# Kernel tuning notes

Hardware: AMD Instinct MI355X
Metric: run time of the kernel (lower is better)

The kernel has to match this reference:

```python
import jax, jax.numpy as jnp
import numpy as np

# ---- static configuration (mirrors init_kwargs) ----
B, V, C, NH, HD = 1, 6, 256, 8, 32     # batch, views, embed, heads, head_dim
Z, L, P = 4, 4, 2                       # z-ref points, fmap levels, ref points
BEV_H, BEV_W = 80, 80
Q = BEV_H * BEV_W
IMG_H, IMG_W = 480, 800
LEVEL_SHAPES = [(60, 100), (30, 50), (15, 25), (8, 13)]
S = sum(h * w for h, w in LEVEL_SHAPES)
RES = 0.512
OFFSET_SCALE = 1.0
FF = 512


def layer_norm(x, g, b):
    m = jnp.mean(x, -1, keepdims=True)
    v = jnp.var(x, -1, keepdims=True)
    return (x - m) / jnp.sqrt(v + 1e-5) * g + b


def _bev_grid():
    xs = (jnp.arange(BEV_W) + 0.5) / BEV_W
    ys = (jnp.arange(BEV_H) + 0.5) / BEV_H
    gy, gx = jnp.meshgrid(ys, xs, indexing='ij')
    ref = jnp.stack([gx.reshape(-1), gy.reshape(-1)], -1)        # (Q,2) normalized xy
    world = (ref - 0.5) * jnp.array([BEV_W * RES, BEV_H * RES])  # (Q,2) ego-frame meters
    return ref, world


def deform_sample(value, H, W, loc):
    """Bilinear sampling. value: (N, H*W, NH, HD); loc: (N, Qn, NH, PP, 2) in [0,1].
    Returns (N, Qn, NH, PP, HD); out-of-bounds samples contribute zero."""
    v = jnp.moveaxis(value, 2, 1)                                # (N, NH, HW, HD)
    x = loc[..., 0] * W - 0.5
    y = loc[..., 1] * H - 0.5
    x0 = jnp.floor(x); y0 = jnp.floor(y)
    lx, ly = x - x0, y - y0
    x0 = x0.astype(jnp.int32); y0 = y0.astype(jnp.int32)
    gather = jax.vmap(jax.vmap(lambda vt, it: vt[it]))           # over (N, NH)
    def corner(xi, yi, w):
        ok = ((xi >= 0) & (xi < W) & (yi >= 0) & (yi < H)).astype(value.dtype)
        idx = jnp.clip(yi, 0, H - 1) * W + jnp.clip(xi, 0, W - 1)
        g = gather(v, jnp.moveaxis(idx, 2, 1))                   # (N,NH,Qn,PP,HD)
        return jnp.moveaxis(g, 1, 2) * (w * ok)[..., None]
    return (corner(x0, y0, (1 - lx) * (1 - ly)) + corner(x0 + 1, y0, lx * (1 - ly))
            + corner(x0, y0 + 1, (1 - lx) * ly) + corner(x0 + 1, y0 + 1, lx * ly))


def _forward(bev_queries, bev_histories, multiscale_fmaps, transition_matrices, z_refs,
             cam_proj_matrices, Wv_t, Woff_t, boff_t, Ww_t, bw_t, Wo_t, bo_t, ln1_g, ln1_b,
             Wv_s, Woff_s, boff_s, Ww_s, bw_s, Wo_s, bo_s, ln2_g, ln2_b,
             W1, b1, W2, b2, ln3_g, ln3_b):
    ref, world = _bev_grid()
    q = bev_queries
    # ---------- temporal self-attention (deformable over current + warped history) ----------
    vcur = (q @ Wv_t).reshape(B, Q, NH, HD)
    vhist = (bev_histories @ Wv_t).reshape(B, Q, NH, HD)
    off_t = (q @ Woff_t + boff_t).reshape(B, Q, NH, 2, P, 2) * OFFSET_SCALE
    w_t = jax.nn.softmax((q @ Ww_t + bw_t).reshape(B, Q, NH, 2 * P), -1).reshape(B, Q, NH, 2, P)
    ext = jnp.array([BEV_W * RES, BEV_H * RES], jnp.float32)
    wh = jnp.concatenate([world, jnp.ones((Q, 1), jnp.float32)], -1)     # (Q,3)
    warped = jnp.einsum('bij,qj->bqi', transition_matrices, wh)          # (B,Q,3)
    ref_hist = warped[..., :2] / warped[..., 2:3] / ext + 0.5            # (B,Q,2)
    norm_bev = jnp.array([BEV_W, BEV_H], jnp.float32)
    loc_c = ref[None, :, None, None, :] + off_t[:, :, :, 0] / norm_bev
    loc_h = ref_hist[:, :, None, None, :] + off_t[:, :, :, 1] / norm_bev
    s_c = deform_sample(vcur, BEV_H, BEV_W, loc_c)                       # (B,Q,NH,P,HD)
    s_h = deform_sample(vhist, BEV_H, BEV_W, loc_h)
    out_t = (jnp.einsum('bqhp,bqhpd->bqhd', w_t[:, :, :, 0], s_c)
             + jnp.einsum('bqhp,bqhpd->bqhd', w_t[:, :, :, 1], s_h))
    out1 = out_t.reshape(B, Q, C) @ Wo_t + bo_t
    out2 = layer_norm(out1 + q, ln1_g, ln1_b)
    # ---------- spatial cross-attention (multi-view multi-scale deformable) ----------
    val = (multiscale_fmaps @ Wv_s).reshape(B * V, S, NH, HD)
    pts = jnp.concatenate([
        jnp.broadcast_to(world[:, None, :], (Q, Z, 2)),
        jnp.broadcast_to(z_refs[None, :, None], (Q, Z, 1)),
        jnp.ones((Q, Z, 1), jnp.float32)], -1)                           # (Q,Z,4) homogeneous
    uvd = jnp.einsum('vij,qzj->vqzi', cam_proj_matrices, pts)            # (V,Q,Z,3)
    d = uvd[..., 2]
    un = uvd[..., 0] / jnp.maximum(d, 1e-5) / IMG_W
    vn = uvd[..., 1] / jnp.maximum(d, 1e-5) / IMG_H
    valid = ((d > 1e-5) & (un >= 0) & (un <= 1) & (vn >= 0) & (vn <= 1)).astype(q.dtype)
    refuv = jnp.stack([un, vn], -1)                                      # (V,Q,Z,2)
    off_s = (out2 @ Woff_s + boff_s).reshape(B, Q, NH, Z, L, P, 2) * OFFSET_SCALE
    w_s = jax.nn.softmax((out2 @ Ww_s + bw_s).reshape(B, Q, NH, Z * L * P), -1)
    w_s = w_s.reshape(B, Q, NH, Z, L, P)
    acc = jnp.zeros((B, Q, NH, HD), q.dtype)
    start = 0
    for l, (Hl, Wl) in enumerate(LEVEL_SHAPES):
        vl = val[:, start:start + Hl * Wl]
        start += Hl * Wl
        loc = (refuv[None, :, :, None, :, None, :]
               + off_s[:, None, :, :, :, l] / jnp.array([Wl, Hl], jnp.float32))
        loc = jnp.broadcast_to(loc, (B, V, Q, NH, Z, P, 2)).reshape(B * V, Q, NH, Z * P, 2)
        samp = deform_sample(vl, Hl, Wl, loc).reshape(B, V, Q, NH, Z, P, HD)
        wl = w_s[:, None, :, :, :, l] * valid[None, :, :, None, :, None]
        acc = acc + jnp.einsum('bvqhzp,bvqhzpd->bqhd', wl, samp)
    count = jnp.maximum(valid.sum((0, 2)), 1.0)                          # (Q,) hit count
    out3 = (acc / count[None, :, None, None]).reshape(B, Q, C) @ Wo_s + bo_s
    out4 = layer_norm(out3 + out2, ln2_g, ln2_b)
    # ---------- feed-forward ----------
    out5 = jax.nn.relu(out4 @ W1 + b1) @ W2 + b2
    return layer_norm(out5 + out4, ln3_g, ln3_b)


def setup_inputs() -> dict:
    key = jax.random.key(0)
    ks = iter(jax.random.split(key, 40))
    def rn(shape, s=1.0):
        return jax.random.normal(next(ks), shape, jnp.float32) * s
    sc = 1.0 / float(np.sqrt(C))
    inp = {}
    inp['bev_queries'] = rn((B, Q, C), 0.1)
    inp['bev_histories'] = rn((B, Q, C), 0.1)
    inp['multiscale_fmaps'] = rn((B, V, S, C), 0.1)
    th = 0.02
    T = np.array([[np.cos(th), -np.sin(th), 0.5],
                  [np.sin(th), np.cos(th), 0.1],
                  [0.0, 0.0, 1.0]], np.float32)
    inp['transition_matrices'] = jnp.tile(jnp.asarray(T)[None], (B, 1, 1))
    inp['z_refs'] = jnp.linspace(-5.0, 3.0, Z).astype(jnp.float32)
    K = np.array([[400.0, 0.0, IMG_W / 2], [0.0, 400.0, IMG_H / 2], [0.0, 0.0, 1.0]], np.float32)
    Ps = []
    for vi in range(V):
        a = 2 * np.pi * vi / V
        Rt = np.zeros((3, 4), np.float32)
        Rt[0, :3] = [-np.sin(a), np.cos(a), 0.0]   # camera right
        Rt[1, :3] = [0.0, 0.0, -1.0]               # camera down
        Rt[2, :3] = [np.cos(a), np.sin(a), 0.0]    # camera forward
        Ps.append(K @ Rt)
    inp['cam_proj_matrices'] = jnp.asarray(np.stack(Ps))
    # temporal self-attention params
    inp['Wv_t'] = rn((C, C), sc)
    inp['Woff_t'] = rn((C, NH * 2 * P * 2), sc * 0.1)
    inp['boff_t'] = jnp.zeros((NH * 2 * P * 2,), jnp.float32)
    inp['Ww_t'] = rn((C, NH * 2 * P), sc)
    inp['bw_t'] = jnp.zeros((NH * 2 * P,), jnp.float32)
    inp['Wo_t'] = rn((C, C), sc)
    inp['bo_t'] = jnp.zeros((C,), jnp.float32)
    inp['ln1_g'] = jnp.ones((C,), jnp.float32)
    inp['ln1_b'] = jnp.zeros((C,), jnp.float32)
    # spatial cross-attention params
    inp['Wv_s'] = rn((C, C), sc)
    inp['Woff_s'] = rn((C, NH * Z * L * P * 2), sc * 0.1)
    inp['boff_s'] = jnp.zeros((NH * Z * L * P * 2,), jnp.float32)
    inp['Ww_s'] = rn((C, NH * Z * L * P), sc)
    inp['bw_s'] = jnp.zeros((NH * Z * L * P,), jnp.float32)
    inp['Wo_s'] = rn((C, C), sc)
    inp['bo_s'] = jnp.zeros((C,), jnp.float32)
    inp['ln2_g'] = jnp.ones((C,), jnp.float32)
    inp['ln2_b'] = jnp.zeros((C,), jnp.float32)
    # FFN params
    inp['W1'] = rn((C, FF), sc)
    inp['b1'] = jnp.zeros((FF,), jnp.float32)
    inp['W2'] = rn((FF, C), 1.0 / float(np.sqrt(FF)))
    inp['b2'] = jnp.zeros((C,), jnp.float32)
    inp['ln3_g'] = jnp.ones((C,), jnp.float32)
    inp['ln3_b'] = jnp.zeros((C,), jnp.float32)
    # static shape descriptors (treated as compile-time constants)
    inp['bev_spatial_shape'] = np.array([[BEV_H, BEV_W]], np.int64)
    inp['multiscale_fmap_shapes'] = np.array(LEVEL_SHAPES, np.int64)
    inp['img_spatial_shape'] = np.array([[IMG_H, IMG_W]], np.int64)
    return inp


def reference(bev_queries, bev_histories, multiscale_fmaps, transition_matrices, z_refs,
              cam_proj_matrices, Wv_t, Woff_t, boff_t, Ww_t, bw_t, Wo_t, bo_t, ln1_g, ln1_b,
              Wv_s, Woff_s, boff_s, Ww_s, bw_s, Wo_s, bo_s, ln2_g, ln2_b,
              W1, b1, W2, b2, ln3_g, ln3_b,
              bev_spatial_shape, multiscale_fmap_shapes, img_spatial_shape):
    return _forward(bev_queries, bev_histories, multiscale_fmaps, transition_matrices, z_refs,
                    cam_proj_matrices, Wv_t, Woff_t, boff_t, Ww_t, bw_t, Wo_t, bo_t, ln1_g, ln1_b,
                    Wv_s, Woff_s, boff_s, Ww_s, bw_s, Wo_s, bo_s, ln2_g, ln2_b,
                    W1, b1, W2, b2, ln3_g, ln3_b)
```

## Files before the change

kernel.cpp:

```cpp
#include <hip/hip_runtime.h>
#include <hip/hip_bf16.h>
#include <hip/hip_fp16.h>

typedef unsigned short u16;
typedef unsigned int u32;
typedef __attribute__((ext_vector_type(8))) short bf16x8;
typedef __attribute__((ext_vector_type(4))) float f32x4;

#define Q_N  6400
#define S_N  7979
#define BEV  80

__device__ __forceinline__ float ubf(u16 u) {
    return __uint_as_float(((u32)u) << 16);
}
__device__ __forceinline__ u16 bfrn(float x) {
    u32 b = __float_as_uint(x);
    return (u16)((b + 0x7FFFu + ((b >> 16) & 1u)) >> 16);
}
__device__ __forceinline__ float f16tof(u16 u) {
    __half h; *(u16*)&h = u; return __half2float(h);
}
__device__ __forceinline__ u16 ftof16(float f) {
    __half h = __float2half(f); return *(u16*)&h;
// ... 1 lines not shown

template <int AIN, int RELU, int OUTMODE, int SM4, int SM32>
__device__ __forceinline__ void gemm_body(
    const void* __restrict__ A, const u16* __restrict__ WhT, const u16* __restrict__ WlT,
    const float* __restrict__ bias, const float* __restrict__ bias2,
    void* __restrict__ Cout, int M, int N, int K, int bx, int by,
    u16* Ah, u16* Al, u16* Wh, u16* Wl)
{
    const int tid  = threadIdx.x;
    const int lane = tid & 63;
    const int wave = tid >> 6;
    const int wm = (wave >> 1) * 32, wn = (wave & 1) * 64;
    const int m0 = by * 64, n0 = bx * 128;
    const int arow = tid >> 2, ak = (tid & 3) * 8;
    const int wrow = tid >> 1, wk = (tid & 1) * 16;
    const int fr = lane & 15, g = lane >> 4;

    f32x4 acc[8];
    #pragma unroll
    for (int i = 0; i < 8; ++i) acc[i] = (f32x4)(0.f);

    for (int k0 = 0; k0 < K; k0 += 32) {
        {
            const bool okr = (m0 + arow) < M;
            float vals[8];
            if (AIN == 0) {
                const float* ap = (const float*)A + (size_t)(m0 + arow) * K + k0 + ak;
                float4 v0 = okr ? *(const float4*)(ap)     : make_float4(0.f, 0.f, 0.f, 0.f);
                float4 v1 = okr ? *(const float4*)(ap + 4) : make_float4(0.f, 0.f, 0.f, 0.f);
                vals[0] = v0.x; vals[1] = v0.y; vals[2] = v0.z; vals[3] = v0.w;
                vals[4] = v1.x; vals[5] = v1.y; vals[6] = v1.z; vals[7] = v1.w;
// ... 1 lines not shown
                const u16* ap = (const u16*)A + (size_t)(m0 + arow) * K + k0 + ak;
                uint4 u = okr ? *(const uint4*)ap : make_uint4(0, 0, 0, 0);
                const __half2* hp = (const __half2*)&u;
                #pragma unroll
                for (int i = 0; i < 4; ++i) {
                    float2 f = __half22float2(hp[i]);
                    vals[2 * i] = f.x; vals[2 * i + 1] = f.y;
                }
            }
            u16 hb[8], lb[8];
            #pragma unroll
            for (int i = 0; i < 8; ++i) {
                hb[i] = bfrn(vals[i]);
                lb[i] = bfrn(vals[i] - ubf(hb[i]));
            }
            u16* dh = &Ah[arow * 40 + ak];
            u16* dl = &Al[arow * 40 + ak];
            *(ushort4*)(dh)     = *(ushort4*)&hb[0];
            *(ushort4*)(dh + 4) = *(ushort4*)&hb[4];
            *(ushort4*)(dl)     = *(ushort4*)&lb[0];
            *(ushort4*)(dl + 4) = *(ushort4*)&lb[4];
        }
        {
            const size_t wo = (size_t)(n0 + wrow) * K + k0 + wk;
            *(uint4*)&Wh[wrow * 40 + wk]     = *(const uint4*)(WhT + wo);
            *(uint4*)&Wh[wrow * 40 + wk + 8] = *(const uint4*)(WhT + wo + 8);
            *(uint4*)&Wl[wrow * 40 + wk]     = *(const uint4*)(WlT + wo);
            *(uint4*)&Wl[wrow * 40 + wk + 8] = *(const uint4*)(WlT + wo + 8);
        }
        __syncthreads();
        bf16x8 fah[2], fal[2], fwh[4], fwl[4];
        #pragma unroll
        for (int i = 0; i < 2; ++i) {
            fah[i] = *(const bf16x8*)&Ah[(wm + i * 16 + fr) * 40 + g * 8];
            fal[i] = *(const bf16x8*)&Al[(wm + i * 16 + fr) * 40 + g * 8];
        }
        #pragma unroll
        for (int j = 0; j < 4; ++j) {
            fwh[j] = *(const bf16x8*)&Wh[(wn + j * 16 + fr) * 40 + g * 8];
            fwl[j] = *(const bf16x8*)&Wl[(wn + j * 16 + fr) * 40 + g * 8];
        }
        #pragma unroll
        for (int i = 0; i < 2; ++i)
            #pragma unroll
            for (int j = 0; j < 4; ++j) {
                acc[i * 4 + j] = __builtin_amdgcn_mfma_f32_16x16x32_bf16(fah[i], fwh[j], acc[i * 4 + j], 0, 0, 0);
                acc[i * 4 + j] = __builtin_amdgcn_mfma_f32_16x16x32_bf16(fal[i], fwh[j], acc[i * 4 + j], 0, 0, 0);
                acc[i * 4 + j] = __builtin_amdgcn_mfma_f32_16x16x32_bf16(fah[i], fwl[j], acc[i * 4 + j], 0, 0, 0);
            }
        __syncthreads();
    }
    const int g4r = g * 4;
    float bv[4];
    #pragma unroll
    for (int j = 0; j < 4; ++j) {
        int col = n0 + wn + j * 16 + fr;
        if (bias2) bv[j] = (col < 512) ? bias[col] : bias2[col - 512];
        else       bv[j] = bias ? bias[col] : 0.f;
    }
    const bool do_sm32 = SM32 && ((n0 + wn) >= 512);
    const bool do_sm4  = SM4 && (wn == 64);
    #pragma unroll
    for (int i = 0; i < 2; ++i) {
        #pragma unroll
        for (int r = 0; r < 4; ++r) {
            const int row = m0 + wm + i * 16 + g4r + r;
            float v0 = acc[i * 4 + 0][r] + bv[0];
// ... 55 lines not shown
                    cp[colb + 16] = ftof16(v1);
                    cp[colb + 32] = ftof16(v2);
                    cp[colb + 48] = ftof16(v3);
                } else {
                    float* cp = (float*)Cout + (size_t)row * N;
                    cp[colb]      = v0;
                    cp[colb + 16] = v1;
                    cp[colb + 32] = v2;
                    cp[colb + 48] = v3;
                }
            }
        }
    }
}

template <int AIN, int RELU, int OUTMODE, int SM32>
__global__ __launch_bounds__(256) void mgemm_k(
    const void* __restrict__ A, const u16* __restrict__ WhT, const u16* __restrict__ WlT,
    const float* __restrict__ bias, const float* __restrict__ bias2,
    void* __restrict__ Cout, int M, int N, int K)
{
    __shared__ u16 Ah[64 * 40], Al[64 * 40], Wh[128 * 40], Wl[128 * 40];
    gemm_body<AIN, RELU, OUTMODE, 0, SM32>(A, WhT, WlT, bias, bias2, Cout,
                                           M, N, K, blockIdx.x, blockIdx.y, Ah, Al, Wh, Wl);
}

__global__ __launch_bounds__(256) void fused3_k(
    const float* __restrict__ fmaps, const float* __restrict__ q, const float* __restrict__ hist,
    const u16* __restrict__ Wv_s_h, const u16* __restrict__ Wv_s_l,
    const u16* __restrict__ Wv_t_h, const u16* __restrict__ Wv_t_l,
    const u16* __restrict__ Wc_h,   const u16* __restrict__ Wc_l,
    const float* __restrict__ bc,
    u16* __restrict__ val_f16, u16* __restrict__ vcur, u16* __restrict__ vhist,
    float* __restrict__ owt)
{
    __shared__ u16 Ah[64 * 40], Al[64 * 40], Wh[128 * 40], Wl[128 * 40];
    const int b = blockIdx.x;
    if (b < 1498) {
        gemm_body<0, 0, 1, 0, 0>(fmaps, Wv_s_h, Wv_s_l, nullptr, nullptr, val_f16,
                                 47874, 256, 256, b & 1, b >> 1, Ah, Al, Wh, Wl);
    } else if (b < 1698) {
        int l = b - 1498;
        gemm_body<0, 0, 1, 0, 0>(q, Wv_t_h, Wv_t_l, nullptr, nullptr, vcur,
                                 6400, 256, 256, l & 1, l >> 1, Ah, Al, Wh, Wl);
    } else if (b < 1898) {
        int l = b - 1698;
        gemm_body<0, 0, 1, 0, 0>(hist, Wv_t_h, Wv_t_l, nullptr, nullptr, vhist,
                                 6400, 256, 256, l & 1, l >> 1, Ah, Al, Wh, Wl);
    } else {
        int l = b - 1898;
        gemm_body<0, 0, 0, 1, 0>(q, Wc_h, Wc_l, bc, nullptr, owt,
                                 6400, 128, 256, 0, l, Ah, Al, Wh, Wl);
    }
}

__global__ __launch_bounds__(256) void wprep_k(
    const float* __restrict__ w0, const float* __restrict__ w1, const float* __restrict__ w2,
    const float* __restrict__ w3, const float* __restrict__ w4, const float* __restrict__ w5,
    const float* __restrict__ w6, const float* __restrict__ w7, u16* __restrict__ base,
    const float* __restrict__ Woff_t, const float* __restrict__ Ww_t,
    const float* __restrict__ boff_t, const float* __restrict__ bw_t,
    float* __restrict__ bc)
{
    const int b = blockIdx.x, tid = threadIdx.x;
    if (b == 184) {
        if (tid < 128) bc[tid] = (tid < 64) ? boff_t[tid] : (tid < 96 ? bw_t[tid - 64] : 0.f);
        return;
// ... 38 lines not shown
    for (int i = 0; i < 16; ++i) {
        float v = tile[kc + i][nr];
        hb[i] = bfrn(v);
        lb[i] = bfrn(v - ubf(hb[i]));
    }
    u16* hp = base + hoff[seg] + (size_t)(n0 + nr) * K + k0 + kc;
    u16* lp = base + loff[seg] + (size_t)(n0 + nr) * K + k0 + kc;
    *(ushort4*)(hp + 0)  = *(ushort4*)&hb[0];
    *(ushort4*)(hp + 4)  = *(ushort4*)&hb[4];
    *(ushort4*)(hp + 8)  = *(ushort4*)&hb[8];
    *(ushort4*)(hp + 12) = *(ushort4*)&hb[12];
    *(ushort4*)(lp + 0)  = *(ushort4*)&lb[0];
    *(ushort4*)(lp + 4)  = *(ushort4*)&lb[4];
    *(ushort4*)(lp + 8)  = *(ushort4*)&lb[8];
    *(ushort4*)(lp + 12) = *(ushort4*)&lb[12];
}

__global__ __launch_bounds__(256) void ln_k(
    const float* __restrict__ x, const float* __restrict__ res,
    const float* __restrict__ g, const float* __restrict__ b,
    float* __restrict__ out)
{
    const int row = blockIdx.x, t = threadIdx.x;
    const size_t idx = (size_t)row * 256 + t;
    float v = x[idx] + res[idx];
    float s = v, ss = v * v;
    #pragma unroll
    for (int o = 32; o > 0; o >>= 1) {
        s += __shfl_down(s, o);
        ss += __shfl_down(ss, o);
    }
    __shared__ float red[8];
    __shared__ float mv[2];
    const int wv = t >> 6, ln = t & 63;
    if (ln == 0) { red[wv] = s; red[4 + wv] = ss; }
    __syncthreads();
    if (t == 0) {
        float S = red[0] + red[1] + red[2] + red[3];
        float SS = red[4] + red[5] + red[6] + red[7];
        float mean = S * (1.f / 256.f);
        float var = SS * (1.f / 256.f) - mean * mean;
        mv[0] = mean;
        mv[1] = rsqrtf(var + 1e-5f);
    }
    __syncthreads();
    out[idx] = (v - mv[0]) * mv[1] * g[t] + b[t];
}

__device__ __forceinline__ float4 bilin4h(const u16* __restrict__ v, int H, int W,
                                          float x, float y, int chb)
{
    float xf = floorf(x), yf = floorf(y);
    int x0 = (int)xf, y0 = (int)yf;
    int x1 = x0 + 1, y1 = y0 + 1;
    float fx = x - xf, fy = y - yf;
    float w00 = (1.f - fx) * (1.f - fy), w10 = fx * (1.f - fy);
    float w01 = (1.f - fx) * fy,         w11 = fx * fy;
    bool xi0 = (x0 >= 0) && (x0 < W);
    bool xi1 = (x1 >= 0) && (x1 < W);
    bool yi0 = (y0 >= 0) && (y0 < H);
    bool yi1 = (y1 >= 0) && (y1 < H);
// ... 4 lines not shown
            float2 f0 = __half22float2(*(const __half2*)&u.x);                   \
            float2 f1 = __half22float2(*(const __half2*)&u.y);                   \
            r.x += (ww) * f0.x; r.y += (ww) * f0.y;                              \
            r.z += (ww) * f1.x; r.w += (ww) * f1.y;                              \
        }
    CORNER(xi0, yi0, x0, y0, w00)
    CORNER(xi1, yi0, x1, y0, w10)
    CORNER(xi0, yi1, x0, y1, w01)
    CORNER(xi1, yi1, x1, y1, w11)
    #undef CORNER
    return r;
}

__global__ __launch_bounds__(256) void temporal_k(
    const u16* __restrict__ vcur, const u16* __restrict__ vhist,
    const float* __restrict__ ow,
    const float* __restrict__ Tm, float* __restrict__ outt)
{
    const int b = blockIdx.x;
    const int q = (b & 7) * 800 + (b >> 3);
    const int tid = threadIdx.x;
    const int c4 = tid & 63, rep = tid >> 6;
    const int br = rep >> 1, p = rep & 1;
    const int h = c4 >> 3;
    const int chb = h * 32 + (c4 & 7) * 4;
    const int jx = q % BEV, iy = q / BEV;
    const float refx = (jx + 0.5f) / 80.f;
    const float refy = (iy + 0.5f) / 80.f;
    const float wx = (refx - 0.5f) * 40.96f;
    const float wy = (refy - 0.5f) * 40.96f;
    float bx, by;
    const u16* v;
// ... 20 lines not shown
        float4 o = make_float4(a.x + b2.x + c.x + d.x, a.y + b2.y + c.y + d.y,
                               a.z + b2.z + c.z + d.z, a.w + b2.w + c.w + d.w);
        *(float4*)(outt + (size_t)q * 256 + c4 * 4) = o;
    }
}

__global__ __launch_bounds__(256) void spatial_k(
    const u16* __restrict__ val, const u16* __restrict__ ow,
    const float* __restrict__ cam, const float* __restrict__ zrefs,
    float* __restrict__ out)
{
    const int b = blockIdx.x;
    const int q = (b & 7) * 800 + (b >> 3);
    const int tid = threadIdx.x;
    const int lane = tid & 63, wave = tid >> 6;
    const int hw = lane >> 5, lh = lane & 31;
    const int slot = wave * 2 + hw;
    const int h = lh >> 2, chb = h * 32 + (lh & 3) * 8;
    __shared__ float s_un[24], s_vn[24], s_ok[24];
    __shared__ int s_list[24];
    __shared__ int s_n;
    __shared__ float s_cnt;
    __shared__ float s_ox[256], s_oy[256], s_wt[256];
    __shared__ float s_part[8][256];
    const int jx = q % BEV, iy = q / BEV;
    const float wx = ((jx + 0.5f) / 80.f - 0.5f) * 40.96f;
    const float wy = ((iy + 0.5f) / 80.f - 0.5f) * 40.96f;
    if (tid < 24) {
        int v = tid >> 2, zz = tid & 3;
        float zr = zrefs[zz];
        const float* P = cam + v * 12;
        float u0 = P[0] * wx + P[1] * wy + P[2] * zr + P[3];
        float u1 = P[4] * wx + P[5] * wy + P[6] * zr + P[7];
        float dd = P[8] * wx + P[9] * wy + P[10] * zr + P[11];
        float dm = fmaxf(dd, 1e-5f);
        float un = u0 / dm / 800.f;
        float vn = u1 / dm / 480.f;
        bool ok = (dd > 1e-5f) && (un >= 0.f) && (un <= 1.f) && (vn >= 0.f) && (vn <= 1.f);
        s_un[tid] = un; s_vn[tid] = vn; s_ok[tid] = ok ? 1.f : 0.f;
    }
    {
        const u16* owq = ow + (size_t)q * 768;
        #pragma unroll
        for (int rep = 0; rep < 2; ++rep) {
            int flat = tid + rep * 256;
            int hh = flat >> 6, rem = flat & 63;
            int zz = rem >> 4, ll = (rem >> 2) & 3, pp = (rem >> 1) & 1, xy = rem & 1;
            int dst = (zz * 8 + ll * 2 + pp) * 8 + hh;
            float v = f16tof(owq[flat]);
            if (xy) s_oy[dst] = v; else s_ox[dst] = v;
        }
        int hh = tid >> 5, rem = tid & 31;
        s_wt[rem * 8 + hh] = f16tof(owq[512 + tid]);
    }
    __syncthreads();
    if (tid == 0) {
        int n = 0; float c = 0.f;
        for (int vz = 0; vz < 24; ++vz) {
            if (s_ok[vz] != 0.f) { s_list[n++] = vz; c += 1.f; }
        }
        s_n = n; s_cnt = fmaxf(c, 1.f);
    }
    __syncthreads();
    const int n = s_n;
    const int LH[4] = {60, 30, 15, 8};
    const int LW[4] = {100, 50, 25, 13};
    const int LS[4] = {0, 6000, 7500, 7875};
    float a0 = 0.f, a1 = 0.f, a2 = 0.f, a3 = 0.f, a4 = 0.f, a5 = 0.f, a6 = 0.f, a7 = 0.f;
    for (int it = slot; it < n; it += 8) {
        int vz = s_list[it];
        int v = vz >> 2, z = vz & 3;
        float un = s_un[vz], vn = s_vn[vz];
        #pragma unroll
        for (int l = 0; l < 4; ++l) {
            const int Hl = LH[l], Wl = LW[l];
            const u16* lv = val + ((size_t)v * S_N + LS[l]) * 256 + chb;
            const float unl = un * Wl - 0.5f, vnl = vn * Hl - 0.5f;
            #pragma unroll
            for (int p = 0; p < 2; ++p) {
                int idx = (z * 8 + l * 2 + p) * 8 + h;
                float x = unl + s_ox[idx];
                float y = vnl + s_oy[idx];
                float wgt = s_wt[idx];
                float xf = floorf(x), yf = floorf(y);
                int x0 = (int)xf, y0 = (int)yf;
                float fx = x - xf, fy = y - yf;
                __half2 w00 = __float2half2_rn((1.f - fx) * (1.f - fy) * wgt);
                __half2 w10 = __float2half2_rn(fx * (1.f - fy) * wgt);
                __half2 w01 = __float2half2_rn((1.f - fx) * fy * wgt);
                __half2 w11 = __float2half2_rn(fx * fy * wgt);
                bool xi0 = (x0 >= 0) && (x0 < Wl);
                bool xi1 = (x0 + 1 >= 0) && (x0 + 1 < Wl);
                bool yi0 = (y0 >= 0) && (y0 < Hl);
                bool yi1 = (y0 + 1 >= 0) && (y0 + 1 < Hl);
                const u16* r0p = lv + (size_t)y0 * (Wl * 256);
                const u16* r1p = r0p + (size_t)(Wl * 256);
                __half2 h0 = __float2half2_rn(0.f), h1 = h0, h2 = h0, h3 = h0;
                if (yi0 && xi0) {
                    uint4 u = *(const uint4*)(r0p + (size_t)x0 * 256);
                    const __half2* hp = (const __half2*)&u;
                    h0 = __hfma2(w00, hp[0], h0); h1 = __hfma2(w00, hp[1], h1);
                    h2 = __hfma2(w00, hp[2], h2); h3 = __hfma2(w00, hp[3], h3);
                }
                if (yi0 && xi1) {
                    uint4 u = *(const uint4*)(r0p + (size_t)(x0 + 1) * 256);
                    const __half2* hp = (const __half2*)&u;
                    h0 = __hfma2(w10, hp[0], h0); h1 = __hfma2(w10, hp[1], h1);
                    h2 = __hfma2(w10, hp[2], h2); h3 = __hfma2(w10, hp[3], h3);
                }
                if (yi1 && xi0) {
                    uint4 u = *(const uint4*)(r1p + (size_t)x0 * 256);
                    const __half2* hp = (const __half2*)&u;
                    h0 = __hfma2(w01, hp[0], h0); h1 = __hfma2(w01, hp[1], h1);
                    h2 = __hfma2(w01, hp[2], h2); h3 = __hfma2(w01, hp[3], h3);
                }
                if (yi1 && xi1) {
                    uint4 u = *(const uint4*)(r1p + (size_t)(x0 + 1) * 256);
                    const __half2* hp = (const __half2*)&u;
                    h0 = __hfma2(w11, hp[0], h0); h1 = __hfma2(w11, hp[1], h1);
                    h2 = __hfma2(w11, hp[2], h2); h3 = __hfma2(w11, hp[3], h3);
                }
                float2 f0 = __half22float2(h0), f1 = __half22float2(h1);
                float2 f2 = __half22float2(h2), f3 = __half22float2(h3);
                a0 += f0.x; a1 += f0.y; a2 += f1.x; a3 += f1.y;
                a4 += f2.x; a5 += f2.y; a6 += f3.x; a7 += f3.y;
            }
        }
    }
    *(float4*)&s_part[slot][chb]     = make_float4(a0, a1, a2, a3);
    *(float4*)&s_part[slot][chb + 4] = make_float4(a4, a5, a6, a7);
    __syncthreads();
    float sum = 0.f;
    #pragma unroll
    for (int k = 0; k < 8; ++k) sum += s_part[k][tid];
    out[(size_t)q * 256 + tid] = sum / s_cnt;
}

extern "C" void kernel_launch(void* const* d_in, const int* in_sizes, int n_in,
                              void* d_out, int out_size, void* d_ws, size_t ws_size,
                              hipStream_t stream) {
    (void)in_sizes; (void)n_in; (void)out_size; (void)ws_size;
    const float* q      = (const float*)d_in[0];
    const float* hist   = (const float*)d_in[1];
    const float* fmaps  = (const float*)d_in[2];
    const float* Tm     = (const float*)d_in[3];
    const float* zrefs  = (const float*)d_in[4];
    const float* cam    = (const float*)d_in[5];
    const float* Woff_t = (const float*)d_in[7];
    const float* boff_t = (const float*)d_in[8];
// ... 1 lines not shown
    const float* bw_t   = (const float*)d_in[10];
    const float* bo_t   = (const float*)d_in[12];
    const float* ln1g   = (const float*)d_in[13];
    const float* ln1b   = (const float*)d_in[14];
    const float* boff_s = (const float*)d_in[17];
    const float* bw_s   = (const float*)d_in[19];
    const float* bo_s   = (const float*)d_in[21];
    const float* ln2g   = (const float*)d_in[22];
    const float* ln2b   = (const float*)d_in[23];
    const float* b1     = (const float*)d_in[25];
    const float* b2     = (const float*)d_in[27];
    const float* ln3g   = (const float*)d_in[28];
    const float* ln3b   = (const float*)d_in[29];

    float* ws    = (float*)d_ws;
    float* r0    = ws;
    float* r1    = ws + 1638400;
    float* owt   = ws + 3276800;
    float* r4    = ws + 4096000;
    u16*  r5u    = (u16*)(ws + 5734400);
    float* of4   = ws + 8192000;
    u16*  valbuf = (u16*)(ws + 9830400);
    u16*  vcur   = (u16*)(ws + 15958272);
    u16*  vhist  = (u16*)(ws + 16777472);
    u16*  wtab   = (u16*)(ws + 17596672);
    float* bc    = ws + 18350336;

    u16* hidden = valbuf;
    u16* Wv_t_h = wtab + 0,       *Wv_t_l = wtab + 65536;
    u16* Wo_t_h = wtab + 131072,  *Wo_t_l = wtab + 196608;
    u16* Wv_s_h = wtab + 262144,  *Wv_s_l = wtab + 327680;
    u16* Comb_h = wtab + 393216,  *Comb_l = wtab + 589824;
    u16* Wo_s_h = wtab + 786432,  *Wo_s_l = wtab + 851968;
    u16* W1_h   = wtab + 917504,  *W1_l   = wtab + 1048576;
    u16* W2_h   = wtab + 1179648, *W2_l   = wtab + 1310720;
    u16* Wc_h   = wtab + 1441792, *Wc_l   = wtab + 1474560;

    dim3 blk(256);
    auto gm = [](int M, int N) { return dim3((unsigned)(N / 128), (unsigned)((M + 63) / 64)); };

    wprep_k<<<dim3(185), blk, 0, stream>>>(
        (const float*)d_in[6], (const float*)d_in[11], (const float*)d_in[15],
        (const float*)d_in[16], (const float*)d_in[18], (const float*)d_in[20],
        (const float*)d_in[24], (const float*)d_in[26], wtab,
        Woff_t, Ww_t, boff_t, bw_t, bc);
    fused3_k<<<dim3(1998), blk, 0, stream>>>(
        fmaps, q, hist, Wv_s_h, Wv_s_l, Wv_t_h, Wv_t_l, Wc_h, Wc_l, bc,
        valbuf, vcur, vhist, owt);
    temporal_k<<<dim3(6400), blk, 0, stream>>>(vcur, vhist, owt, Tm, r4);
    mgemm_k<0,0,0,0><<<gm(6400, 256), blk, 0, stream>>>(
        r4, Wo_t_h, Wo_t_l, bo_t, nullptr, r0, 6400, 256, 256);
    ln_k<<<dim3(6400), blk, 0, stream>>>(r0, q, ln1g, ln1b, r1);
    mgemm_k<0,0,1,1><<<gm(6400, 768), blk, 0, stream>>>(
        r1, Comb_h, Comb_l, boff_s, bw_s, r5u, 6400, 768, 256);
    spatial_k<<<dim3(6400), blk, 0, stream>>>(valbuf, r5u, cam, zrefs, r0);
    mgemm_k<0,0,0,0><<<gm(6400, 256), blk, 0, stream>>>(
        r0, Wo_s_h, Wo_s_l, bo_s, nullptr, r4, 6400, 256, 256);
    ln_k<<<dim3(6400), blk, 0, stream>>>(r4, r1, ln2g, ln2b, of4);
    mgemm_k<0,1,1,0><<<gm(6400, 512), blk, 0, stream>>>(
        of4, W1_h, W1_l, b1, nullptr, hidden, 6400, 512, 256);
    mgemm_k<1,0,0,0><<<gm(6400, 256), blk, 0, stream>>>(
        hidden, W2_h, W2_l, b2, nullptr, r0, 6400, 256, 512);
    ln_k<<<dim3(6400), blk, 0, stream>>>(r0, of4, ln3g, ln3b, (float*)d_out);
}
```

Before: 351.2 us.

## Fuse residual+LayerNorm into full-width GEMMs and use head-major value layout for sampling

Adds a 64x256-tile GEMM body that covers all 256 output columns per block, so bias, residual add and LayerNorm can be done in the epilogue. This removes the three separate ln_k launches and their intermediate round trips. The value projection now writes a head-major (view, head, pixel, channel) fp16 layout. spatial_k is rewritten so each lane group handles one head, fetching two vertical corners per x-selector lane with float accumulation. The trade-off is fewer blocks per GEMM (100 instead of 200) and more shared memory per block, which can reduce occupancy.

Measured after the change: 396.7 us. 13.0% more time.

```diff
diff --git a/kernel.cpp b/kernel.cpp
--- a/kernel.cpp
+++ b/kernel.cpp
@@ -39,7 +39,7 @@
     const int m0 = by * 64, n0 = bx * 128;
     const int arow = tid >> 2, ak = (tid & 3) * 8;
     const int wrow = tid >> 1, wk = (tid & 1) * 16;
-    const int fr = lane & 15, g = lane >> 4;
+    const int fr = lane & 15, gq = lane >> 4;
 
     f32x4 acc[8];
     #pragma unroll
@@ -71,12 +71,10 @@
                 hb[i] = bfrn(vals[i]);
                 lb[i] = bfrn(vals[i] - ubf(hb[i]));
             }
-            u16* dh = &Ah[arow * 40 + ak];
-            u16* dl = &Al[arow * 40 + ak];
-            *(ushort4*)(dh)     = *(ushort4*)&hb[0];
-            *(ushort4*)(dh + 4) = *(ushort4*)&hb[4];
-            *(ushort4*)(dl)     = *(ushort4*)&lb[0];
-            *(ushort4*)(dl + 4) = *(ushort4*)&lb[4];
+            *(ushort4*)(&Ah[arow * 40 + ak])     = *(ushort4*)&hb[0];
+            *(ushort4*)(&Ah[arow * 40 + ak + 4]) = *(ushort4*)&hb[4];
+            *(ushort4*)(&Al[arow * 40 + ak])     = *(ushort4*)&lb[0];
+            *(ushort4*)(&Al[arow * 40 + ak + 4]) = *(ushort4*)&lb[4];
         }
         {
             const size_t wo = (size_t)(n0 + wrow) * K + k0 + wk;
@@ -89,13 +87,13 @@
         bf16x8 fah[2], fal[2], fwh[4], fwl[4];
         #pragma unroll
         for (int i = 0; i < 2; ++i) {
-            fah[i] = *(const bf16x8*)&Ah[(wm + i * 16 + fr) * 40 + g * 8];
-            fal[i] = *(const bf16x8*)&Al[(wm + i * 16 + fr) * 40 + g * 8];
+            fah[i] = *(const bf16x8*)&Ah[(wm + i * 16 + fr) * 40 + gq * 8];
+            fal[i] = *(const bf16x8*)&Al[(wm + i * 16 + fr) * 40 + gq * 8];
         }
         #pragma unroll
         for (int j = 0; j < 4; ++j) {
-            fwh[j] = *(const bf16x8*)&Wh[(wn + j * 16 + fr) * 40 + g * 8];
-            fwl[j] = *(const bf16x8*)&Wl[(wn + j * 16 + fr) * 40 + g * 8];
+            fwh[j] = *(const bf16x8*)&Wh[(wn + j * 16 + fr) * 40 + gq * 8];
+            fwl[j] = *(const bf16x8*)&Wl[(wn + j * 16 + fr) * 40 + gq * 8];
         }
         #pragma unroll
         for (int i = 0; i < 2; ++i)
@@ -107,7 +105,7 @@
             }
         __syncthreads();
     }
-    const int g4r = g * 4;
+    const int g4r = gq * 4;
     float bv[4];
     #pragma unroll
     for (int j = 0; j < 4; ++j) {
@@ -193,15 +191,194 @@
     }
 }
 
+template <int AIN, int OUTMODE, int LN>
+__device__ __forceinline__ void gemm_body256(
+    const void* __restrict__ A, const u16* __restrict__ WhT, const u16* __restrict__ WlT,
+    const float* __restrict__ bias, const float* __restrict__ res,
+    const float* __restrict__ gam, const float* __restrict__ bet,
+    void* __restrict__ Cout, int M, int K, int by, u16* smem)
+{
+    u16* Ah = smem;
+    u16* Al = smem + 2560;
+    u16* Wh = smem + 5120;
+    u16* Wl = smem + 15360;
+    const int tid  = threadIdx.x;
+    const int lane = tid & 63;
+    const int wave = tid >> 6;
+    const int wm = (wave >> 1) * 32, wn = (wave & 1) * 128;
+    const int m0 = by * 64;
+    const int arow = tid >> 2, ak = (tid & 3) * 8;
+    const int fr = lane & 15, gq = lane >> 4;
+
+    f32x4 acc[16];
+    #pragma unroll
+    for (int i = 0; i < 16; ++i) acc[i] = (f32x4)(0.f);
+
+    for (int k0 = 0; k0 < K; k0 += 32) {
+        {
+            const bool okr = (m0 + arow) < M;
+            float vals[8];
+            if (AIN == 0) {
+                const float* ap = (const float*)A + (size_t)(m0 + arow) * K + k0 + ak;
+                float4 v0 = okr ? *(const float4*)(ap)     : make_float4(0.f, 0.f, 0.f, 0.f);
+                float4 v1 = okr ? *(const float4*)(ap + 4) : make_float4(0.f, 0.f, 0.f, 0.f);
+                vals[0] = v0.x; vals[1] = v0.y; vals[2] = v0.z; vals[3] = v0.w;
+                vals[4] = v1.x; vals[5] = v1.y; vals[6] = v1.z; vals[7] = v1.w;
+            } else {
+                const u16* ap = (const u16*)A + (size_t)(m0 + arow) * K + k0 + ak;
+                uint4 u = okr ? *(const uint4*)ap : make_uint4(0, 0, 0, 0);
+                const __half2* hp = (const __half2*)&u;
+                #pragma unroll
+                for (int i = 0; i < 4; ++i) {
+                    float2 f = __half22float2(hp[i]);
+                    vals[2 * i] = f.x; vals[2 * i + 1] = f.y;
+                }
+            }
+            u16 hb[8], lb[8];
+            #pragma unroll
+            for (int i = 0; i < 8; ++i) {
+                hb[i] = bfrn(vals[i]);
+                lb[i] = bfrn(vals[i] - ubf(hb[i]));
+            }
+            *(ushort4*)(&Ah[arow * 40 + ak])     = *(ushort4*)&hb[0];
+            *(ushort4*)(&Ah[arow * 40 + ak + 4]) = *(ushort4*)&hb[4];
+            *(ushort4*)(&Al[arow * 40 + ak])     = *(ushort4*)&lb[0];
+            *(ushort4*)(&Al[arow * 40 + ak + 4]) = *(ushort4*)&lb[4];
+        }
+        {
+            const size_t wo = (size_t)tid * K + k0;
+            const uint4* sh = (const uint4*)(WhT + wo);
+            const uint4* sl = (const uint4*)(WlT + wo);
+            uint4* dh = (uint4*)&Wh[tid * 40];
+            uint4* dl = (uint4*)&Wl[tid * 40];
+            dh[0] = sh[0]; dh[1] = sh[1]; dh[2] = sh[2]; dh[3] = sh[3];
+            dl[0] = sl[0]; dl[1] = sl[1]; dl[2] = sl[2]; dl[3] = sl[3];
+        }
+        __syncthreads();
+        bf16x8 fah[2], fal[2];
+        #pragma unroll
+        for (int i = 0; i < 2; ++i) {
+            fah[i] = *(const bf16x8*)&Ah[(wm + i * 16 + fr) * 40 + gq * 8];
+            fal[i] = *(const bf16x8*)&Al[(wm + i * 16 + fr) * 40 + gq * 8];
+        }
+        #pragma unroll
+        for (int jg = 0; jg < 2; ++jg) {
+            bf16x8 fwh[4], fwl[4];
+            #pragma unroll
+            for (int j = 0; j < 4; ++j) {
+                fwh[j] = *(const bf16x8*)&Wh[(wn + jg * 64 + j * 16 + fr) * 40 + gq * 8];
+                fwl[j] = *(const bf16x8*)&Wl[(wn + jg * 64 + j * 16 + fr) * 40 + gq * 8];
+            }
+            #pragma unroll
+            for (int i = 0; i < 2; ++i)
+                #pragma unroll
+                for (int j = 0; j < 4; ++j) {
+                    int a = i * 8 + jg * 4 + j;
+                    acc[a] = __builtin_amdgcn_mfma_f32_16x16x32_bf16(fah[i], fwh[j], acc[a], 0, 0, 0);
+                    acc[a] = __builtin_amdgcn_mfma_f32_16x16x32_bf16(fal[i], fwh[j], acc[a], 0, 0, 0);
+                    acc[a] = __builtin_amdgcn_mfma_f32_16x16x32_bf16(fah[i], fwl[j], acc[a], 0, 0, 0);
+                }
+        }
+        __syncthreads();
+    }
+    const int g4r = gq * 4;
+    if (LN) {
+        u16* lnbuf = smem;
+        float* sred = (float*)(smem + 16384);
+        #pragma unroll
+        for (int i = 0; i < 2; ++i) {
+            #pragma unroll
+            for (int r = 0; r < 4; ++r) {
+                const int rl = wm + i * 16 + g4r + r;
+                const int row = m0 + rl;
+                float s = 0.f, ss = 0.f;
+                #pragma unroll
+                for (int j = 0; j < 8; ++j) {
+                    int col = wn + j * 16 + fr;
+                    float v = acc[i * 8 + j][r] + bias[col] + res[(size_t)row * 256 + col];
+                    s += v; ss += v * v;
+                    lnbuf[rl * 256 + col] = ftof16(v);
+                }
+                s += __shfl_xor(s, 1); ss += __shfl_xor(ss, 1);
+                s += __shfl_xor(s, 2); ss += __shfl_xor(ss, 2);
+                s += __shfl_xor(s, 4); ss += __shfl_xor(ss, 4);
+                s += __shfl_xor(s, 8); ss += __shfl_xor(ss, 8);
+                if (fr == 0) {
+                    sred[rl * 2 + (wave & 1)] = s;
+                    sred[128 + rl * 2 + (wave & 1)] = ss;
+                }
+            }
+        }
+        __syncthreads();
+        #pragma unroll
+        for (int i = 0; i < 2; ++i) {
+            #pragma unroll
+            for (int r = 0; r < 4; ++r) {
+                const int rl = wm + i * 16 + g4r + r;
+                const int row = m0 + rl;
+                float S  = sred[rl * 2] + sred[rl * 2 + 1];
+                float SS = sred[128 + rl * 2] + sred[128 + rl * 2 + 1];
+                float mean = S * (1.f / 256.f);
+                float var = SS * (1.f / 256.f) - mean * mean;
+                float rstd = rsqrtf(var + 1e-5f);
+                #pragma unroll
+                for (int j = 0; j < 8; ++j) {
+                    int col = wn + j * 16 + fr;
+                    float v = f16tof(lnbuf[rl * 256 + col]);
+                    ((float*)Cout)[(size_t)row * 256 + col] =
+                        (v - mean) * rstd * gam[col] + bet[col];
+                }
+            }
+        }
+    } else {
+        #pragma unroll
+        for (int i = 0; i < 2; ++i) {
+            #pragma unroll
+            for (int r = 0; r < 4; ++r) {
+                const int row = m0 + wm + i * 16 + g4r + r;
+                if (row >= M) continue;
+                int vi = 0, si = 0;
+                if (OUTMODE == 2) { vi = row / S_N; si = row - vi * S_N; }
+                #pragma unroll
+                for (int j = 0; j < 8; ++j) {
+                    int col = wn + j * 16 + fr;
+                    float v = acc[i * 8 + j][r] + (bias ? bias[col] : 0.f);
+                    if (OUTMODE == 2) {
+                        int hh = col >> 5, cc = col & 31;
+                        ((u16*)Cout)[(((size_t)vi * 8 + hh) * S_N + si) * 32 + cc] = ftof16(v);
+                    } else if (OUTMODE == 1) {
+                        ((u16*)Cout)[(size_t)row * 256 + col] = ftof16(v);
+                    } else {
+                        ((float*)Cout)[(size_t)row * 256 + col] = v;
+                    }
+                }
+            }
+        }
+    }
+}
+
 template <int AIN, int RELU, int OUTMODE, int SM32>
 __global__ __launch_bounds__(256) void mgemm_k(
     const void* __restrict__ A, const u16* __restrict__ WhT, const u16* __restrict__ WlT,
     const float* __restrict__ bias, const float* __restrict__ bias2,
     void* __restrict__ Cout, int M, int N, int K)
 {
-    __shared__ u16 Ah[64 * 40], Al[64 * 40], Wh[128 * 40], Wl[128 * 40];
+    __shared__ u16 smem[15360];
     gemm_body<AIN, RELU, OUTMODE, 0, SM32>(A, WhT, WlT, bias, bias2, Cout,
-                                           M, N, K, blockIdx.x, blockIdx.y, Ah, Al, Wh, Wl);
+                                           M, N, K, blockIdx.x, blockIdx.y,
+                                           smem, smem + 2560, smem + 5120, smem + 10240);
+}
+
+template <int AIN, int OUTMODE, int LN>
+__global__ __launch_bounds__(256) void gemm256_k(
+    const void* __restrict__ A, const u16* __restrict__ WhT, const u16* __restrict__ WlT,
+    const float* __restrict__ bias, const float* __restrict__ res,
+    const float* __restrict__ gam, const float* __restrict__ bet,
+    void* __restrict__ Cout, int M, int K)
+{
+    __shared__ u16 smem[25600];
+    gemm_body256<AIN, OUTMODE, LN>(A, WhT, WlT, bias, res, gam, bet, Cout, M, K,
+                                   blockIdx.y, smem);
 }
 
 __global__ __launch_bounds__(256) void fused3_k(
@@ -210,26 +387,24 @@
     const u16* __restrict__ Wv_t_h, const u16* __restrict__ Wv_t_l,
     const u16* __restrict__ Wc_h,   const u16* __restrict__ Wc_l,
     const float* __restrict__ bc,
-    u16* __restrict__ val_f16, u16* __restrict__ vcur, u16* __restrict__ vhist,
+    u16* __restrict__ val_hm, u16* __restrict__ vcur, u16* __restrict__ vhist,
     float* __restrict__ owt)
 {
-    __shared__ u16 Ah[64 * 40], Al[64 * 40], Wh[128 * 40], Wl[128 * 40];
+    __shared__ u16 smem[25600];
     const int b = blockIdx.x;
-    if (b < 1498) {
-        gemm_body<0, 0, 1, 0, 0>(fmaps, Wv_s_h, Wv_s_l, nullptr, nullptr, val_f16,
-                                 47874, 256, 256, b & 1, b >> 1, Ah, Al, Wh, Wl);
-    } else if (b < 1698) {
-        int l = b - 1498;
-        gemm_body<0, 0, 1, 0, 0>(q, Wv_t_h, Wv_t_l, nullptr, nullptr, vcur,
-                                 6400, 256, 256, l & 1, l >> 1, Ah, Al, Wh, Wl);
-    } else if (b < 1898) {
-        int l = b - 1698;
-        gemm_body<0, 0, 1, 0, 0>(hist, Wv_t_h, Wv_t_l, nullptr, nullptr, vhist,
-                                 6400, 256, 256, l & 1, l >> 1, Ah, Al, Wh, Wl);
+    if (b < 749) {
+        gemm_body256<0, 2, 0>(fmaps, Wv_s_h, Wv_s_l, nullptr, nullptr, nullptr, nullptr,
+                              val_hm, 47874, 256, b, smem);
+    } else if (b < 849) {
+        gemm_body256<0, 1, 0>(q, Wv_t_h, Wv_t_l, nullptr, nullptr, nullptr, nullptr,
+                              vcur, 6400, 256, b - 749, smem);
+    } else if (b < 949) {
+        gemm_body256<0, 1, 0>(hist, Wv_t_h, Wv_t_l, nullptr, nullptr, nullptr, nullptr,
+                              vhist, 6400, 256, b - 849, smem);
     } else {
-        int l = b - 1898;
         gemm_body<0, 0, 0, 1, 0>(q, Wc_h, Wc_l, bc, nullptr, owt,
-                                 6400, 128, 256, 0, l, Ah, Al, Wh, Wl);
+                                 6400, 128, 256, 0, b - 949,
+                                 smem, smem + 2560, smem + 5120, smem + 10240);
     }
 }
 
@@ -298,37 +473,6 @@
     *(ushort4*)(lp + 4)  = *(ushort4*)&lb[4];
     *(ushort4*)(lp + 8)  = *(ushort4*)&lb[8];
     *(ushort4*)(lp + 12) = *(ushort4*)&lb[12];
-}
-
-__global__ __launch_bounds__(256) void ln_k(
-    const float* __restrict__ x, const float* __restrict__ res,
-    const float* __restrict__ g, const float* __restrict__ b,
-    float* __restrict__ out)
-{
-    const int row = blockIdx.x, t = threadIdx.x;
-    const size_t idx = (size_t)row * 256 + t;
-    float v = x[idx] + res[idx];
-    float s = v, ss = v * v;
-    #pragma unroll
-    for (int o = 32; o > 0; o >>= 1) {
-        s += __shfl_down(s, o);
-        ss += __shfl_down(ss, o);
-    }
-    __shared__ float red[8];
-    __shared__ float mv[2];
-    const int wv = t >> 6, ln = t & 63;
-    if (ln == 0) { red[wv] = s; red[4 + wv] = ss; }
-    __syncthreads();
-    if (t == 0) {
-        float S = red[0] + red[1] + red[2] + red[3];
-        float SS = red[4] + red[5] + red[6] + red[7];
-        float mean = S * (1.f / 256.f);
-        float var = SS * (1.f / 256.f) - mean * mean;
-        mv[0] = mean;
-        mv[1] = rsqrtf(var + 1e-5f);
-    }
-    __syncthreads();
-    out[idx] = (v - mv[0]) * mv[1] * g[t] + b[t];
 }
 
 __device__ __forceinline__ float4 bilin4h(const u16* __restrict__ v, int H, int W,
@@ -363,8 +507,7 @@
 
 __global__ __launch_bounds__(256) void temporal_k(
     const u16* __restrict__ vcur, const u16* __restrict__ vhist,
-    const float* __restrict__ ow,
-    const float* __restrict__ Tm, float* __restrict__ outt)
+    const float* __restrict__ ow, const float* __restrict__ Tm, float* __restrict__ outt)
 {
     const int b = blockIdx.x;
     const int q = (b & 7) * 800 + (b >> 3);
@@ -415,25 +558,24 @@
     const int q = (b & 7) * 800 + (b >> 3);
     const int tid = threadIdx.x;
     const int lane = tid & 63, wave = tid >> 6;
-    const int hw = lane >> 5, lh = lane & 31;
-    const int slot = wave * 2 + hw;
-    const int h = lh >> 2, chb = h * 32 + (lh & 3) * 8;
+    const int h = lane >> 3, sub = lane & 7;
+    const int xsel = sub >> 2, c8 = (sub & 3) * 8;
     __shared__ float s_un[24], s_vn[24], s_ok[24];
     __shared__ int s_list[24];
     __shared__ int s_n;
     __shared__ float s_cnt;
     __shared__ float s_ox[256], s_oy[256], s_wt[256];
-    __shared__ float s_part[8][256];
+    __shared__ float s_part[4][256];
     const int jx = q % BEV, iy = q / BEV;
-    const float wx = ((jx + 0.5f) / 80.f - 0.5f) * 40.96f;
-    const float wy = ((iy + 0.5f) / 80.f - 0.5f) * 40.96f;
+    const float wxw = ((jx + 0.5f) / 80.f - 0.5f) * 40.96f;
+    const float wyw = ((iy + 0.5f) / 80.f - 0.5f) * 40.96f;
     if (tid < 24) {
         int v = tid >> 2, zz = tid & 3;
         float zr = zrefs[zz];
         const float* P = cam + v * 12;
-        float u0 = P[0] * wx + P[1] * wy + P[2] * zr + P[3];
-        float u1 = P[4] * wx + P[5] * wy + P[6] * zr + P[7];
-        float dd = P[8] * wx + P[9] * wy + P[10] * zr + P[11];
+        float u0 = P[0] * wxw + P[1] * wyw + P[2] * zr + P[3];
+        float u1 = P[4] * wxw + P[5] * wyw + P[6] * zr + P[7];
+        float dd = P[8] * wxw + P[9] * wyw + P[10] * zr + P[11];
         float dm = fmaxf(dd, 1e-5f);
         float un = u0 / dm / 800.f;
         float vn = u1 / dm / 480.f;
@@ -463,77 +605,57 @@
         s_n = n; s_cnt = fmaxf(c, 1.f);
     }
     __syncthreads();
-    const int n = s_n;
+    const int nu = s_n * 8;
     const int LH[4] = {60, 30, 15, 8};
     const int LW[4] = {100, 50, 25, 13};
     const int LS[4] = {0, 6000, 7500, 7875};
     float a0 = 0.f, a1 = 0.f, a2 = 0.f, a3 = 0.f, a4 = 0.f, a5 = 0.f, a6 = 0.f, a7 = 0.f;
-    for (int it = slot; it < n; it += 8) {
-        int vz = s_list[it];
-        int v = vz >> 2, z = vz & 3;
-        float un = s_un[vz], vn = s_vn[vz];
-        #pragma unroll
-        for (int l = 0; l < 4; ++l) {
-            const int Hl = LH[l], Wl = LW[l];
-            const u16* lv = val + ((size_t)v * S_N + LS[l]) * 256 + chb;
-            const float unl = un * Wl - 0.5f, vnl = vn * Hl - 0.5f;
-            #pragma unroll
-            for (int p = 0; p < 2; ++p) {
-                int idx = (z * 8 + l * 2 + p) * 8 + h;
-                float x = unl + s_ox[idx];
-                float y = vnl + s_oy[idx];
-                float wgt = s_wt[idx];
-                float xf = floorf(x), yf = floorf(y);
-                int x0 = (int)xf, y0 = (int)yf;
-                float fx = x - xf, fy = y - yf;
-                __half2 w00 = __float2half2_rn((1.f - fx) * (1.f - fy) * wgt);
-                __half2 w10 = __float2half2_rn(fx * (1.f - fy) * wgt);
-                __half2 w01 = __float2half2_rn((1.f - fx) * fy * wgt);
-                __half2 w11 = __float2half2_rn(fx * fy * wgt);
-                bool xi0 = (x0 >= 0) && (x0 < Wl);
-                bool xi1 = (x0 + 1 >= 0) && (x0 + 1 < Wl);
-                bool yi0 = (y0 >= 0) && (y0 < Hl);
-                bool yi1 = (y0 + 1 >= 0) && (y0 + 1 < Hl);
-                const u16* r0p = lv + (size_t)y0 * (Wl * 256);
-                const u16* r1p = r0p + (size_t)(Wl * 256);
-                __half2 h0 = __float2half2_rn(0.f), h1 = h0, h2 = h0, h3 = h0;
-                if (yi0 && xi0) {
-                    uint4 u = *(const uint4*)(r0p + (size_t)x0 * 256);
-                    const __half2* hp = (const __half2*)&u;
-                    h0 = __hfma2(w00, hp[0], h0); h1 = __hfma2(w00, hp[1], h1);
-                    h2 = __hfma2(w00, hp[2], h2); h3 = __hfma2(w00, hp[3], h3);
-                }
-                if (yi0 && xi1) {
-                    uint4 u = *(const uint4*)(r0p + (size_t)(x0 + 1) * 256);
-                    const __half2* hp = (const __half2*)&u;
-                    h0 = __hfma2(w10, hp[0], h0); h1 = __hfma2(w10, hp[1], h1);
-                    h2 = __hfma2(w10, hp[2], h2); h3 = __hfma2(w10, hp[3], h3);
-                }
-                if (yi1 && xi0) {
-                    uint4 u = *(const uint4*)(r1p + (size_t)x0 * 256);
-                    const __half2* hp = (const __half2*)&u;
-                    h0 = __hfma2(w01, hp[0], h0); h1 = __hfma2(w01, hp[1], h1);
-                    h2 = __hfma2(w01, hp[2], h2); h3 = __hfma2(w01, hp[3], h3);
-                }
-                if (yi1 && xi1) {
-                    uint4 u = *(const uint4*)(r1p + (size_t)(x0 + 1) * 256);
-                    const __half2* hp = (const __half2*)&u;
-                    h0 = __hfma2(w11, hp[0], h0); h1 = __hfma2(w11, hp[1], h1);
-                    h2 = __hfma2(w11, hp[2], h2); h3 = __hfma2(w11, hp[3], h3);
-                }
-                float2 f0 = __half22float2(h0), f1 = __half22float2(h1);
-                float2 f2 = __half22float2(h2), f3 = __half22float2(h3);
-                a0 += f0.x; a1 += f0.y; a2 += f1.x; a3 += f1.y;
-                a4 += f2.x; a5 += f2.y; a6 += f3.x; a7 += f3.y;
-            }
-        }
-    }
-    *(float4*)&s_part[slot][chb]     = make_float4(a0, a1, a2, a3);
-    *(float4*)&s_part[slot][chb + 4] = make_float4(a4, a5, a6, a7);
+    for (int it = wave; it < nu; it += 4) {
+        const int vz = s_list[it >> 3];
+        const int lp = it & 7, l = lp >> 1, p = lp & 1;
+        const int v = vz >> 2, z = vz & 3;
+        const int Hl = LH[l], Wl = LW[l];
+        const int idx = (z * 8 + l * 2 + p) * 8 + h;
+        float x = s_un[vz] * Wl - 0.5f + s_ox[idx];
+        float y = s_vn[vz] * Hl - 0.5f + s_oy[idx];
+        float wgt = s_wt[idx];
+        float xf = floorf(x), yf = floorf(y);
+        int x0 = (int)xf, y0 = (int)yf;
+        float fx = x - xf, fy = y - yf;
+        int xi = x0 + xsel;
+        float wxc = xsel ? fx : (1.f - fx);
+        if (xi < 0 || xi >= Wl) wxc = 0.f;
+        int xc = min(max(xi, 0), Wl - 1);
+        float wy0 = (y0 >= 0 && y0 < Hl) ? (1.f - fy) : 0.f;
+        float wy1 = (y0 + 1 >= 0 && y0 + 1 < Hl) ? fy : 0.f;
+        int y0c = min(max(y0, 0), Hl - 1);
+        int y1c = min(max(y0 + 1, 0), Hl - 1);
+        const u16* base = val + (((size_t)v * 8 + h) * S_N + LS[l]) * 32 + c8;
+        uint4 u0 = *(const uint4*)(base + ((size_t)y0c * Wl + xc) * 32);
+        uint4 u1 = *(const uint4*)(base + ((size_t)y1c * Wl + xc) * 32);
+        float wA = wgt * wxc * wy0, wB = wgt * wxc * wy1;
+        const __half2* p0 = (const __half2*)&u0;
+        const __half2* p1 = (const __half2*)&u1;
+        float2 f;
+        f = __half22float2(p0[0]); a0 += wA * f.x; a1 += wA * f.y;
+        f = __half22float2(p0[1]); a2 += wA * f.x; a3 += wA * f.y;
+        f = __half22float2(p0[2]); a4 += wA * f.x; a5 += wA * f.y;
+        f = __half22float2(p0[3]); a6 += wA * f.x; a7 += wA * f.y;
+        f = __half22float2(p1[0]); a0 += wB * f.x; a1 += wB * f.y;
+        f = __half22float2(p1[1]); a2 += wB * f.x; a3 += wB * f.y;
+        f = __half22float2(p1[2]); a4 += wB * f.x; a5 += wB * f.y;
+        f = __half22float2(p1[3]); a6 += wB * f.x; a7 += wB * f.y;
+    }
+    a0 += __shfl_xor(a0, 4); a1 += __shfl_xor(a1, 4);
+    a2 += __shfl_xor(a2, 4); a3 += __shfl_xor(a3, 4);
+    a4 += __shfl_xor(a4, 4); a5 += __shfl_xor(a5, 4);
+    a6 += __shfl_xor(a6, 4); a7 += __shfl_xor(a7, 4);
+    if (xsel == 0) {
+        *(float4*)&s_part[wave][h * 32 + c8]     = make_float4(a0, a1, a2, a3);
+        *(float4*)&s_part[wave][h * 32 + c8 + 4] = make_float4(a4, a5, a6, a7);
+    }
     __syncthreads();
-    float sum = 0.f;
-    #pragma unroll
-    for (int k = 0; k < 8; ++k) sum += s_part[k][tid];
+    float sum = s_part[0][tid] + s_part[1][tid] + s_part[2][tid] + s_part[3][tid];
     out[(size_t)q * 256 + tid] = sum / s_cnt;
 }
 
@@ -565,19 +687,19 @@
     const float* ln3b   = (const float*)d_in[29];
 
     float* ws    = (float*)d_ws;
-    float* r0    = ws;
-    float* r1    = ws + 1638400;
-    float* owt   = ws + 3276800;
-    float* r4    = ws + 4096000;
-    u16*  r5u    = (u16*)(ws + 5734400);
-    float* of4   = ws + 8192000;
-    u16*  valbuf = (u16*)(ws + 9830400);
-    u16*  vcur   = (u16*)(ws + 15958272);
-    u16*  vhist  = (u16*)(ws + 16777472);
-    u16*  wtab   = (u16*)(ws + 17596672);
-    float* bc    = ws + 18350336;
-
-    u16* hidden = valbuf;
+    float* r4    = ws;
+    float* out2  = ws + 1638400;
+    float* r0    = ws + 3276800;
+    float* out4  = ws + 4915200;
+    float* owt   = ws + 6553600;
+    u16*  r5u    = (u16*)(ws + 7372800);
+    u16*  valhm  = (u16*)(ws + 9830400);
+    u16*  vcur   = (u16*)(ws + 15958400);
+    u16*  vhist  = (u16*)(ws + 16777600);
+    u16*  wtab   = (u16*)(ws + 17596800);
+    float* bc    = ws + 18350464;
+
+    u16* hidden = valhm;
     u16* Wv_t_h = wtab + 0,       *Wv_t_l = wtab + 65536;
     u16* Wo_t_h = wtab + 131072,  *Wo_t_l = wtab + 196608;
     u16* Wv_s_h = wtab + 262144,  *Wv_s_l = wtab + 327680;
@@ -588,29 +710,25 @@
     u16* Wc_h   = wtab + 1441792, *Wc_l   = wtab + 1474560;
 
     dim3 blk(256);
-    auto gm = [](int M, int N) { return dim3((unsigned)(N / 128), (unsigned)((M + 63) / 64)); };
 
     wprep_k<<<dim3(185), blk, 0, stream>>>(
         (const float*)d_in[6], (const float*)d_in[11], (const float*)d_in[15],
         (const float*)d_in[16], (const float*)d_in[18], (const float*)d_in[20],
         (const float*)d_in[24], (const float*)d_in[26], wtab,
         Woff_t, Ww_t, boff_t, bw_t, bc);
-    fused3_k<<<dim3(1998), blk, 0, stream>>>(
+    fused3_k<<<dim3(1049), blk, 0, stream>>>(
         fmaps, q, hist, Wv_s_h, Wv_s_l, Wv_t_h, Wv_t_l, Wc_h, Wc_l, bc,
-        valbuf, vcur, vhist, owt);
+        valhm, vcur, vhist, owt);
     temporal_k<<<dim3(6400), blk, 0, stream>>>(vcur, vhist, owt, Tm, r4);
-    mgemm_k<0,0,0,0><<<gm(6400, 256), blk, 0, stream>>>(
-        r4, Wo_t_h, Wo_t_l, bo_t, nullptr, r0, 6400, 256, 256);
-    ln_k<<<dim3(6400), blk, 0, stream>>>(r0, q, ln1g, ln1b, r1);
-    mgemm_k<0,0,1,1><<<gm(6400, 768), blk, 0, stream>>>(
-        r1, Comb_h, Comb_l, boff_s, bw_s, r5u, 6400, 768, 256);
-    spatial_k<<<dim3(6400), blk, 0, stream>>>(valbuf, r5u, cam, zrefs, r0);
-    mgemm_k<0,0,0,0><<<gm(6400, 256), blk, 0, stream>>>(
-        r0, Wo_s_h, Wo_s_l, bo_s, nullptr, r4, 6400, 256, 256);
-    ln_k<<<dim3(6400), blk, 0, stream>>>(r4, r1, ln2g, ln2b, of4);
-    mgemm_k<0,1,1,0><<<gm(6400, 512), blk, 0, stream>>>(
-        of4, W1_h, W1_l, b1, nullptr, hidden, 6400, 512, 256);
-    mgemm_k<1,0,0,0><<<gm(6400, 256), blk, 0, stream>>>(
-        hidden, W2_h, W2_l, b2, nullptr, r0, 6400, 256, 512);
-    ln_k<<<dim3(6400), blk, 0, stream>>>(r0, of4, ln3g, ln3b, (float*)d_out);
-}
+    gemm256_k<0,0,1><<<dim3(1, 100), blk, 0, stream>>>(
+        r4, Wo_t_h, Wo_t_l, bo_t, q, ln1g, ln1b, out2, 6400, 256);
+    mgemm_k<0,0,1,1><<<dim3(6, 100), blk, 0, stream>>>(
+        out2, Comb_h, Comb_l, boff_s, bw_s, r5u, 6400, 768, 256);
+    spatial_k<<<dim3(6400), blk, 0, stream>>>(valhm, r5u, cam, zrefs, r0);
+    gemm256_k<0,0,1><<<dim3(1, 100), blk, 0, stream>>>(
+        r0, Wo_s_h, Wo_s_l, bo_s, out2, ln2g, ln2b, out4, 6400, 256);
+    mgemm_k<0,1,1,0><<<dim3(4, 100), blk, 0, stream>>>(
+        out4, W1_h, W1_l, b1, nullptr, hidden, 6400, 512, 256);
+    gemm256_k<1,0,1><<<dim3(1, 100), blk, 0, stream>>>(
+        hidden, W2_h, W2_l, b2, out4, ln3g, ln3b, (float*)d_out, 6400, 512);
+}
```
